# Optimization experiments

Hardware: AMD Instinct MI355X
Metric: run time of the kernel (lower is better)

The kernel has to match this reference:

```python
import jax, jax.numpy as jnp
import numpy as np

N = 50000      # nodes
E = 800000     # edges (avg degree 16)
D = 64         # input_dim
L = 64         # latent_dim


def setup_inputs() -> dict:
    key = jax.random.key(0)
    k1, k2, k3, k4, k5, k6 = jax.random.split(key, 6)
    x = jax.random.normal(k1, (N, D), dtype=jnp.float32)
    weight = jax.random.normal(k2, (D, L), dtype=jnp.float32) / np.sqrt(D)
    bias = jax.random.normal(k3, (L,), dtype=jnp.float32) * 0.01
    # strictly positive degrees to keep division well-behaved
    node_degree = jax.random.uniform(k4, (N, 1), dtype=jnp.float32) + 1.0
    edge_src = jax.random.randint(k5, (E,), 0, N, dtype=jnp.int32)
    edge_dst = jax.random.randint(k6, (E,), 0, N, dtype=jnp.int32)
    return {"x": x, "weight": weight, "bias": bias,
            "node_degree": node_degree,
            "edge_src": edge_src, "edge_dst": edge_dst}


def reference(x, weight, bias, node_degree, edge_src, edge_dst):
    # gnn_spmm(adj, x): sparse aggregate over incoming edges -> [N, D]
    agg = jax.ops.segment_sum(x[edge_src], edge_dst, num_segments=N)
    pooled = agg + x                      # residual self-connection
    node_linear = pooled @ weight + bias  # dense projection [N, L]
    normalized = node_linear / node_degree  # normalize_embedding == 2
    return jax.nn.relu(normalized)
```

## Files before the change

kernel.cpp:

```cpp
#include <hip/hip_runtime.h>
#include <hip/hip_fp16.h>

#define N_NODES 50000
#define DIM 64
#define CB 391
#define PBLK 131
#define PEPB 6144
#define EPT 12
#define RUNW 48
#define CAPB (PBLK * RUNW)
#define BINCAP 64
#define PLW 68

typedef _Float16 half8 __attribute__((ext_vector_type(8)));
typedef _Float16 half4v __attribute__((ext_vector_type(4)));
typedef float floatx4 __attribute__((ext_vector_type(4)));

#define WS_COARSE  0
#define WS_CNT     9834432
#define WS_XH      (WS_CNT + 204928)
#define WS_WT      (WS_XH + 6400000)

__global__ void __launch_bounds__(512) prep_kernel(
        const float* __restrict__ x, const float* __restrict__ W,
        const int* __restrict__ edge_src, const int* __restrict__ edge_dst,
        unsigned int* __restrict__ coarse, int* __restrict__ cnt,
        _Float16* __restrict__ xh, _Float16* __restrict__ wt, int E) {
    int b = blockIdx.x, t = threadIdx.x;
    if (b < PBLK) {
        __shared__ int lhist[CB];
        for (int i = t; i < CB; i += 512) lhist[i] = 0;
        __syncthreads();

        int base = b * PEPB;
        unsigned int pk[EPT];
        int bk[EPT];
        #pragma unroll
        for (int j = 0; j < EPT; ++j) {
            int e = base + j * 512 + t;
            bk[j] = -1;
            if (e < E) {
                int s = edge_src[e];
                int d = edge_dst[e];
                bk[j] = d >> 7;
                pk[j] = ((unsigned int)s << 7) | (unsigned int)(d & 127);
                atomicAdd(&lhist[bk[j]], 1);
            }
        }
        __syncthreads();
        for (int i = t; i < CB; i += 512) {
            cnt[(size_t)b * CB + i] = lhist[i];
            lhist[i] = 0;
        }
        __syncthreads();
        #pragma unroll
        for (int j = 0; j < EPT; ++j) {
            if (bk[j] >= 0) {
                int r = atomicAdd(&lhist[bk[j]], 1);
                coarse[(size_t)bk[j] * CAPB + b * RUNW + r] = pk[j];
            }
        }
    } else if (b < PBLK + 1563) {
        int i = (b - PBLK) * 512 + t;
        if (i < N_NODES * DIM / 4) {
            float4 v = reinterpret_cast<const float4*>(x)[i];
            half4v h = { (_Float16)v.x, (_Float16)v.y, (_Float16)v.z, (_Float16)v.w };
            reinterpret_cast<half4v*>(xh)[i] = h;
        }
    } else {
        #pragma unroll
        for (int i = 0; i < 8; ++i) {
            int idx = t * 8 + i;
            int n = idx >> 6, k = idx & 63;
            wt[idx] = (_Float16)W[k * DIM + n];
        }
    }
}

__global__ void __launch_bounds__(256) fused_kernel(
        const _Float16* __restrict__ xh,
        const _Float16* __restrict__ wt,
        const float* __restrict__ bias,
        const float* __restrict__ deg,
        const int* __restrict__ cnt,
        const unsigned int* __restrict__ coarse,
        float* __restrict__ out) {
    __shared__ unsigned short sedges[64 * BINCAP];
    __shared__ float pl[64 * PLW];
    __shared__ int cur[64];

    int t = threadIdx.x;
    int b = blockIdx.x;
    int bucket = (b >> 4) * 8 + (b & 7);
    int half = (b >> 3) & 1;
    if (bucket >= CB) return;
    int nb = bucket * 128 + half * 64;

    if (t < 64) cur[t] = 0;
    __syncthreads();

    if (t < PBLK) {
        int ci = cnt[(size_t)t * CB + bucket];
        const unsigned int* rp = coarse + (size_t)bucket * CAPB + t * RUNW;
        for (int r = 0; r < ci; ++r) {
            unsigned int e = rp[r];
            int loc = (int)(e & 127u);
            if ((loc >> 6) == half) {
                int bin = loc & 63;
                int p = atomicAdd(&cur[bin], 1);
                sedges[bin * BINCAP + p] = (unsigned short)(e >> 7);
            }
        }
    }
    __syncthreads();

    int g = t >> 3;
    int c = t & 7;
    #pragma unroll
    for (int pass = 0; pass < 2; ++pass) {
        int loc = g + pass * 32;
        int node = nb + loc;
        float acc[8];
        #pragma unroll
        for (int j = 0; j < 8; ++j) acc[j] = 0.f;
        const unsigned short* bp = &sedges[loc * BINCAP];
        int ct = cur[loc];
        int k = 0;
        for (; k + 8 <= ct; k += 8) {
            int sid[8];
            #pragma unroll
            for (int u = 0; u < 8; ++u) sid[u] = (int)bp[k + u];
            half8 v[8];
            #pragma unroll
            for (int u = 0; u < 8; ++u)
                v[u] = *reinterpret_cast<const half8*>(xh + (size_t)sid[u] * DIM + c * 8);
            #pragma unroll
            for (int u = 0; u < 8; ++u) {
                #pragma unroll
                for (int j = 0; j < 8; ++j) acc[j] += (float)v[u][j];
            }
        }
        for (; k + 4 <= ct; k += 4) {
            int sid[4];
            #pragma unroll
            for (int u = 0; u < 4; ++u) sid[u] = (int)bp[k + u];
            half8 v[4];
            #pragma unroll
            for (int u = 0; u < 4; ++u)
                v[u] = *reinterpret_cast<const half8*>(xh + (size_t)sid[u] * DIM + c * 8);
            #pragma unroll
            for (int u = 0; u < 4; ++u) {
                #pragma unroll
                for (int j = 0; j < 8; ++j) acc[j] += (float)v[u][j];
            }
        }
        for (; k < ct; ++k) {
            int s0 = (int)bp[k];
            half8 v0 = *reinterpret_cast<const half8*>(xh + (size_t)s0 * DIM + c * 8);
            #pragma unroll
            for (int j = 0; j < 8; ++j) acc[j] += (float)v0[j];
        }
        if (node < N_NODES) {
            half8 r = *reinterpret_cast<const half8*>(xh + (size_t)node * DIM + c * 8);
            float* p = &pl[loc * PLW + c * 8];
            #pragma unroll
            for (int j = 0; j < 8; ++j) p[j] = acc[j] + (float)r[j];
        }
    }
    __syncthreads();

    int wv = t >> 6;
    int lane = t & 63;
    int m = lane & 15;
    int q = lane >> 4;
    int lbase = wv * 16;

    const float* ap = &pl[(lbase + m) * PLW];
    half8 a0, a1;
    #pragma unroll
    for (int j = 0; j < 8; ++j) a0[j] = (_Float16)ap[q * 8 + j];
    #pragma unroll
    for (int j = 0; j < 8; ++j) a1[j] = (_Float16)ap[32 + q * 8 + j];

    floatx4 acc4[4];
    #pragma unroll
    for (int tt = 0; tt < 4; ++tt) {
        half8 b0 = *reinterpret_cast<const half8*>(wt + (size_t)(tt * 16 + m) * DIM + q * 8);
        half8 b1 = *reinterpret_cast<const half8*>(wt + (size_t)(tt * 16 + m) * DIM + q * 8 + 32);
        floatx4 cfrag = {0.f, 0.f, 0.f, 0.f};
        cfrag = __builtin_amdgcn_mfma_f32_16x16x32_f16(a0, b0, cfrag, 0, 0, 0);
        cfrag = __builtin_amdgcn_mfma_f32_16x16x32_f16(a1, b1, cfrag, 0, 0, 0);
        acc4[tt] = cfrag;
    }

    #pragma unroll
    for (int r = 0; r < 4; ++r) {
        int row = q * 4 + r;
        int node = nb + lbase + row;
        if (node < N_NODES) {
            float inv = 1.0f / deg[node];
            #pragma unroll
            for (int tt = 0; tt < 4; ++tt) {
                float v = (acc4[tt][r] + bias[tt * 16 + m]) * inv;
                out[(size_t)node * DIM + tt * 16 + m] = fmaxf(v, 0.f);
            }
        }
    }
}

extern "C" void kernel_launch(void* const* d_in, const int* in_sizes, int n_in,
                              void* d_out, int out_size, void* d_ws, size_t ws_size,
                              hipStream_t stream) {
    const float* x        = (const float*)d_in[0];
    const float* weight   = (const float*)d_in[1];
    const float* bias     = (const float*)d_in[2];
    const float* node_deg = (const float*)d_in[3];
    const int*   edge_src = (const int*)d_in[4];
    const int*   edge_dst = (const int*)d_in[5];
    float* out = (float*)d_out;
    int E = in_sizes[4];

    char* ws = (char*)d_ws;
    unsigned int* coarse = (unsigned int*)(ws + WS_COARSE);
    int*          cnt    = (int*)(ws + WS_CNT);
    _Float16*     xh     = (_Float16*)(ws + WS_XH);
    _Float16*     wt     = (_Float16*)(ws + WS_WT);

    prep_kernel<<<PBLK + 1563 + 1, 512, 0, stream>>>(
        x, weight, edge_src, edge_dst, coarse, cnt, xh, wt, E);

    fused_kernel<<<784, 256, 0, stream>>>(
        xh, wt, bias, node_deg, cnt, coarse, out);
}
```

Before: 114.7 us.

## Process whole 128-node bucket per 512-thread block with strided edge scatter

Each fused block now handles a full 128-node bucket with 512 threads instead of splitting it into two 64-node halves. Edge loading becomes a coalesced strided loop over the bucket's whole capacity, checked against per-run counts cached in shared memory. Previously 131 threads walked their runs serially and half the edges were discarded. This removes the duplicate coarse-list reads and the serial per-thread loops, at the cost of fewer blocks (391), more shared memory per block, and iterating over empty capacity slots.

```diff
diff --git a/kernel.cpp b/kernel.cpp
--- a/kernel.cpp
+++ b/kernel.cpp
@@ -77,7 +77,7 @@
     }
 }
 
-__global__ void __launch_bounds__(256) fused_kernel(
+__global__ void __launch_bounds__(512) fused_kernel(
         const _Float16* __restrict__ xh,
         const _Float16* __restrict__ wt,
         const float* __restrict__ bias,
@@ -85,31 +85,29 @@
         const int* __restrict__ cnt,
         const unsigned int* __restrict__ coarse,
         float* __restrict__ out) {
-    __shared__ unsigned short sedges[64 * BINCAP];
-    __shared__ float pl[64 * PLW];
-    __shared__ int cur[64];
+    __shared__ unsigned short sedges[128 * BINCAP];
+    __shared__ float pl[128 * PLW];
+    __shared__ int cur[128];
+    __shared__ int lcnt[PBLK];
 
     int t = threadIdx.x;
-    int b = blockIdx.x;
-    int bucket = (b >> 4) * 8 + (b & 7);
-    int half = (b >> 3) & 1;
-    if (bucket >= CB) return;
-    int nb = bucket * 128 + half * 64;
-
-    if (t < 64) cur[t] = 0;
+    int bucket = blockIdx.x;
+    int nb = bucket * 128;
+
+    if (t < 128) cur[t] = 0;
+    if (t >= 128 && t < 128 + PBLK)
+        lcnt[t - 128] = cnt[(size_t)(t - 128) * CB + bucket];
     __syncthreads();
 
-    if (t < PBLK) {
-        int ci = cnt[(size_t)t * CB + bucket];
-        const unsigned int* rp = coarse + (size_t)bucket * CAPB + t * RUNW;
-        for (int r = 0; r < ci; ++r) {
-            unsigned int e = rp[r];
+    const unsigned int* cbk = coarse + (size_t)bucket * CAPB;
+    for (int i = t; i < CAPB; i += 512) {
+        int run = i / RUNW;
+        int r = i - run * RUNW;
+        if (r < lcnt[run]) {
+            unsigned int e = cbk[i];
             int loc = (int)(e & 127u);
-            if ((loc >> 6) == half) {
-                int bin = loc & 63;
-                int p = atomicAdd(&cur[bin], 1);
-                sedges[bin * BINCAP + p] = (unsigned short)(e >> 7);
-            }
+            int p = atomicAdd(&cur[loc], 1);
+            sedges[loc * BINCAP + p] = (unsigned short)(e >> 7);
         }
     }
     __syncthreads();
@@ -118,7 +116,7 @@
     int c = t & 7;
     #pragma unroll
     for (int pass = 0; pass < 2; ++pass) {
-        int loc = g + pass * 32;
+        int loc = g + pass * 64;
         int node = nb + loc;
         float acc[8];
         #pragma unroll
@@ -229,6 +227,6 @@
     prep_kernel<<<PBLK + 1563 + 1, 512, 0, stream>>>(
         x, weight, edge_src, edge_dst, coarse, cnt, xh, wt, E);
 
-    fused_kernel<<<784, 256, 0, stream>>>(
+    fused_kernel<<<CB, 512, 0, stream>>>(
         xh, wt, bias, node_deg, cnt, coarse, out);
 }
```

Result: faster. 112.4 us (-2.0%).
